# Optimization experiments

Measured on AMD Instinct MI355X. Metric: run time of the kernel, lower is better.

## Reference

```python
import jax, jax.numpy as jnp
import numpy as np

B = 512      # batch
T = 32       # time steps -> T-1 = 31 recurrent steps
Tm1 = T - 1
D = 256      # input_size (exogenous features)
HE = 512     # encoder hidden
HD = 512     # decoder hidden


def setup_inputs() -> dict:
    key = jax.random.key(0)
    ks = jax.random.split(key, 24)
    n = lambda k, shape, s=0.05: jax.random.normal(k, shape, dtype=jnp.float32) * s
    return dict(
        inputs=jax.random.normal(ks[0], (B, Tm1, D + 1), dtype=jnp.float32),
        enc_Wih=n(ks[1], (4 * HE, D)), enc_Whh=n(ks[2], (4 * HE, HE)),
        enc_bih=n(ks[3], (4 * HE,)), enc_bhh=n(ks[4], (4 * HE,)),
        enc_Wc=n(ks[5], (Tm1, 2 * HE)), enc_bc=n(ks[6], (Tm1,)),
        enc_Wd=n(ks[7], (Tm1, Tm1)), enc_bd=n(ks[8], (Tm1,)),
        enc_Wa=n(ks[9], (1, Tm1)), enc_ba=n(ks[10], (1,)),
        dec_W1=n(ks[11], (HE, 2 * HD + HE)), dec_b1=n(ks[12], (HE,)),
        dec_W2=n(ks[13], (1, HE)), dec_b2=n(ks[14], (1,)),
        dec_Wih=n(ks[15], (4 * HD, 1)), dec_Whh=n(ks[16], (4 * HD, HD)),
        dec_bih=n(ks[17], (4 * HD,)), dec_bhh=n(ks[18], (4 * HD,)),
        fc_W=n(ks[19], (1, HE + 1), 1.0),  # torch code does fc.weight.data.normal_() (std=1)
        fc_b=n(ks[20], (1,)),
        fcf_W=n(ks[21], (1, HD + HE)), fcf_b=n(ks[22], (1,)),
    )


def _lstm_step(x, h, c, Wih, Whh, bih, bhh):
    # single-step PyTorch LSTM; gate order i, f, g, o
    g = x @ Wih.T + bih + h @ Whh.T + bhh
    i, f, gg, o = jnp.split(g, 4, axis=-1)
    c2 = jax.nn.sigmoid(f) * c + jax.nn.sigmoid(i) * jnp.tanh(gg)
    return jax.nn.sigmoid(o) * jnp.tanh(c2), c2


def reference(inputs, enc_Wih, enc_Whh, enc_bih, enc_bhh, enc_Wc, enc_bc,
              enc_Wd, enc_bd, enc_Wa, enc_ba, dec_W1, dec_b1, dec_W2, dec_b2,
              dec_Wih, dec_Whh, dec_bih, dec_bhh, fc_W, fc_b, fcf_W, fcf_b):
    Bn = inputs.shape[0]
    y_hist = inputs[:, :, :1]   # idx_target = 0 -> [B, Tm1, 1]
    X = inputs[:, :, 1:]        # [B, Tm1, D]

    # linear_data(input_data.permute(0,2,1)) is time-invariant: [B, D, Tm1]
    t2 = jnp.einsum('btd,st->bds', X, enc_Wd) + enc_bd

    # ---- Encoder: input attention + LSTM over Tm1 steps ----
    def enc_step(carry, x_t):
        h, c = carry  # [B, HE] each
        # hidden/state are identical per input feature -> compute linear_concat once
        t1 = jnp.concatenate([h, c], axis=-1) @ enc_Wc.T + enc_bc        # [B, Tm1]
        score = jnp.tanh(t1[:, None, :] + t2) @ enc_Wa[0] + enc_ba[0]     # [B, D]
        attn = jax.nn.softmax(score, axis=1)
        w = attn * x_t                                                    # [B, D]
        h2, c2 = _lstm_step(w, h, c, enc_Wih, enc_Whh, enc_bih, enc_bhh)
        return (h2, c2), h2

    h0 = jnp.zeros((Bn, HE), dtype=inputs.dtype)
    (_, _), enc_h = jax.lax.scan(enc_step, (h0, h0), jnp.swapaxes(X, 0, 1))
    enc_out = jnp.swapaxes(enc_h, 0, 1)  # [B, Tm1, HE]

    # ---- Decoder: temporal attention + LSTM over Tm1 steps ----
    def dec_step(carry, y_t):
        h, c, _ = carry
        hs = jnp.concatenate([h, c], axis=-1)  # [B, 2*HD]
        x = jnp.concatenate(
            [jnp.broadcast_to(hs[:, None, :], (Bn, Tm1, 2 * HD)), enc_out], axis=-1)
        score = jnp.tanh(x @ dec_W1.T + dec_b1) @ dec_W2[0] + dec_b2[0]   # [B, Tm1]
        a = jax.nn.softmax(score, axis=1)
        ctx = jnp.einsum('bt,bte->be', a, enc_out)                        # [B, HE]
        y_tilde = jnp.concatenate([ctx, y_t], axis=-1) @ fc_W.T + fc_b    # [B, 1]
        h2, c2 = _lstm_step(y_tilde, h, c, dec_Wih, dec_Whh, dec_bih, dec_bhh)
        return (h2, c2, ctx), None

    hd0 = jnp.zeros((Bn, HD), dtype=inputs.dtype)
    ctx0 = jnp.zeros((Bn, HE), dtype=inputs.dtype)
    (hT, _, ctxT), _ = jax.lax.scan(dec_step, (hd0, hd0, ctx0),
                                    jnp.swapaxes(y_hist, 0, 1))
    return jnp.concatenate([hT, ctxT], axis=-1) @ fcf_W.T + fcf_b  # [B, 1]
```

## Files before the change

### kernel.cpp

```cpp
#include <hip/hip_runtime.h>
#include <math.h>

#define BATCH 512
#define TM1   31
#define DIMD  256

typedef _Float16 f16;
typedef _Float16 half2v __attribute__((ext_vector_type(2)));
typedef _Float16 half8 __attribute__((ext_vector_type(8)));
typedef float floatx16 __attribute__((ext_vector_type(16)));

__device__ __forceinline__ float sigmf(float x) { return 1.f / (1.f + __expf(-x)); }

__device__ __forceinline__ float tanh_fast(float x) {
    float ax = fabsf(x);
    float t  = __expf(-2.f * ax);
    float r  = (1.f - t) / (1.f + t);
    return copysignf(r, x);
}

__device__ __forceinline__ float blockReduceSum256(float v, float* sred) {
#pragma unroll
    for (int m = 32; m > 0; m >>= 1) v += __shfl_xor(v, m);
    __syncthreads();
    if ((threadIdx.x & 63) == 0) sred[threadIdx.x >> 6] = v;
    __syncthreads();
    return sred[0] + sred[1] + sred[2] + sred[3];
}

__device__ __forceinline__ float blockReduceMax256(float v, float* sred) {
#pragma unroll
    for (int m = 32; m > 0; m >>= 1) v = fmaxf(v, __shfl_xor(v, m));
    __syncthreads();
    if ((threadIdx.x & 63) == 0) sred[threadIdx.x >> 6] = v;
    __syncthreads();
    return fmaxf(fmaxf(sred[0], sred[1]), fmaxf(sred[2], sred[3]));
}

__global__ __launch_bounds__(256) void prep_t2s_kernel(
    const float* __restrict__ inputs,
    const float* __restrict__ eWih, const float* __restrict__ eWhh,
    const float* __restrict__ ebih, const float* __restrict__ ebhh,
    const float* __restrict__ dW1,  const float* __restrict__ dWhh,
    const float* __restrict__ dbih, const float* __restrict__ dbhh,
    const float* __restrict__ Wd,   const float* __restrict__ bd,
    const float* __restrict__ Wc,
    f16* __restrict__ eWf, f16* __restrict__ dWcf, f16* __restrict__ Vwf,
    float* __restrict__ ebcomb, float* __restrict__ dbias,
    f16* __restrict__ t2s, f16* __restrict__ Wcf)
{
    __shared__ float sX[TM1 * DIMD];
    __shared__ float sWd[TM1 * TM1];
    int b = blockIdx.x, tid = threadIdx.x;
    int idx = b * 256 + tid;
    const int stride = 512 * 256;

    for (int i = tid; i < TM1 * DIMD; i += 256) {
        int tt = i >> 8, d = i & 255;
        sX[i] = inputs[((size_t)b * TM1 + tt) * 257 + 1 + d];
    }
    for (int i = tid; i < TM1 * TM1; i += 256) sWd[i] = Wd[i];
    __syncthreads();
    int d = tid;
    for (int s = 0; s < TM1; s++) {
        float acc = bd[s];
        for (int tt = 0; tt < TM1; tt++) acc += sX[tt * DIMD + d] * sWd[s * TM1 + tt];
        t2s[((size_t)b * TM1 + s) * DIMD + d] = (f16)acc;
    }

    for (int g = idx; g < 2048 * 96; g += stride) {
        int n = g / 96, k0 = (g % 96) * 8;
        const float* src = (k0 < 256) ? (eWih + n * 256 + k0)
                                      : (eWhh + n * 512 + (k0 - 256));
        float4 v0 = *(const float4*)src;
        float4 v1 = *(const float4*)(src + 4);
        f16 h[8] = {(f16)v0.x, (f16)v0.y, (f16)v0.z, (f16)v0.w,
                    (f16)v1.x, (f16)v1.y, (f16)v1.z, (f16)v1.w};
        *(half8*)(eWf + n * 768 + k0) = *(half8*)h;
    }
    for (int g = idx; g < 2560 * 128; g += stride) {
        int n = g >> 7, k0 = (g & 127) * 8;
        float vv[8] = {};
        if (n < 512) {
            const float* src = dW1 + n * 1536 + k0;
            float4 v0 = *(const float4*)src, v1 = *(const float4*)(src + 4);
            vv[0]=v0.x; vv[1]=v0.y; vv[2]=v0.z; vv[3]=v0.w;
            vv[4]=v1.x; vv[5]=v1.y; vv[6]=v1.z; vv[7]=v1.w;
        } else if (k0 < 512) {
            const float* src = dWhh + (n - 512) * 512 + k0;
            float4 v0 = *(const float4*)src, v1 = *(const float4*)(src + 4);
            vv[0]=v0.x; vv[1]=v0.y; vv[2]=v0.z; vv[3]=v0.w;
            vv[4]=v1.x; vv[5]=v1.y; vv[6]=v1.z; vv[7]=v1.w;
        }
        f16 h[8];
#pragma unroll
        for (int e = 0; e < 8; e++) h[e] = (f16)vv[e];
        *(half8*)(dWcf + n * 1024 + k0) = *(half8*)h;
    }
    for (int g = idx; g < 512 * 64; g += stride) {
        int n = g >> 6, k0 = (g & 63) * 8;
        const float* src = dW1 + n * 1536 + 1024 + k0;
        float4 v0 = *(const float4*)src, v1 = *(const float4*)(src + 4);
        f16 h[8] = {(f16)v0.x, (f16)v0.y, (f16)v0.z, (f16)v0.w,
                    (f16)v1.x, (f16)v1.y, (f16)v1.z, (f16)v1.w};
        *(half8*)(Vwf + n * 512 + k0) = *(half8*)h;
    }
    for (int g = idx; g < 3968; g += stride) {
        int k0 = g * 8;
        float4 v0 = *(const float4*)(Wc + k0);
        float4 v1 = *(const float4*)(Wc + k0 + 4);
        f16 h[8] = {(f16)v0.x, (f16)v0.y, (f16)v0.z, (f16)v0.w,
                    (f16)v1.x, (f16)v1.y, (f16)v1.z, (f16)v1.w};
        *(half8*)(Wcf + k0) = *(half8*)h;
    }
    for (int i = idx; i < 2048; i += stride) ebcomb[i] = ebih[i] + ebhh[i];
    for (int i = idx; i < 2560; i += stride)
        dbias[i] = (i < 512) ? 0.f : (dbih[i - 512] + dbhh[i - 512]);
}

__global__ __launch_bounds__(256) void gemm1f(
    const f16* __restrict__ A, int lda,
    const f16* __restrict__ W, int ldw,
    const float* __restrict__ bias, f16* __restrict__ C, int ldc,
    long long Cstride, int K, int nsplit, int NT, int MT, int KS)
{
    __shared__ f16 sAh[64 * 128];
    __shared__ f16 sWh[64 * 128];
    int tid = threadIdx.x, bid = blockIdx.x;
    int nbase = bid % NT;
    int m0 = ((bid / NT) % MT) * 64;
    int ks = bid / (NT * MT);
    int lane = tid & 63, wid = tid >> 6;
    int wm = wid >> 1, wn = wid & 1;
    int rl = lane & 31, kq = lane >> 5;

    int sr = tid >> 2;
    int gb = (tid & 3) * 4;
    int st0 = sr * 128 + (((gb + 0) ^ (sr & 15)) * 8);
    int st1 = sr * 128 + (((gb + 1) ^ (sr & 15)) * 8);
    int st2 = sr * 128 + (((gb + 2) ^ (sr & 15)) * 8);
    int st3 = sr * 128 + (((gb + 3) ^ (sr & 15)) * 8);
    int arow = (wm * 32 + rl) * 128;
    int wrow = (wn * 32 + rl) * 128;
    int swk = rl & 15;

    int n0 = nbase * 64;
    int Kfull = (n0 >= nsplit) ? 512 : K;
    int ksz = Kfull / KS;
    int kbeg = ks * ksz, kend = kbeg + ksz;

    const f16* pA = A + (size_t)(m0 + sr) * lda + gb * 8;
    const f16* pW = W + (size_t)(n0 + sr) * ldw + gb * 8;

    float4 rA0 = *(const float4*)(pA + kbeg);
    float4 rA1 = *(const float4*)(pA + kbeg + 8);
    float4 rA2 = *(const float4*)(pA + kbeg + 16);
    float4 rA3 = *(const float4*)(pA + kbeg + 24);
    float4 rW0 = *(const float4*)(pW + kbeg);
    float4 rW1 = *(const float4*)(pW + kbeg + 8);
    float4 rW2 = *(const float4*)(pW + kbeg + 16);
    float4 rW3 = *(const float4*)(pW + kbeg + 24);

    floatx16 acc = {};
    for (int k0 = kbeg; k0 < kend; k0 += 128) {
        __syncthreads();
        *(float4*)&sAh[st0] = rA0; *(float4*)&sAh[st1] = rA1;
        *(float4*)&sAh[st2] = rA2; *(float4*)&sAh[st3] = rA3;
        *(float4*)&sWh[st0] = rW0; *(float4*)&sWh[st1] = rW1;
        *(float4*)&sWh[st2] = rW2; *(float4*)&sWh[st3] = rW3;
        __syncthreads();
        int kn = k0 + 128;
        if (kn < kend) {
            rA0 = *(const float4*)(pA + kn);      rA1 = *(const float4*)(pA + kn + 8);
            rA2 = *(const float4*)(pA + kn + 16); rA3 = *(const float4*)(pA + kn + 24);
            rW0 = *(const float4*)(pW + kn);      rW1 = *(const float4*)(pW + kn + 8);
            rW2 = *(const float4*)(pW + kn + 16); rW3 = *(const float4*)(pW + kn + 24);
        }
#pragma unroll
        for (int kk = 0; kk < 128; kk += 16) {
            int lg = (kk >> 3) + kq;
            half8 ah = *(const half8*)&sAh[arow + ((lg ^ swk) * 8)];
            half8 wh = *(const half8*)&sWh[wrow + ((lg ^ swk) * 8)];
            acc = __builtin_amdgcn_mfma_f32_32x32x16_f16(ah, wh, acc, 0, 0, 0);
        }
    }

    int col = n0 + wn * 32 + rl;
    float bv = (ks == 0) ? bias[col] : 0.f;
    f16* Cp = C + (size_t)ks * Cstride;
#pragma unroll
    for (int rr = 0; rr < 16; ++rr) {
        int row = m0 + wm * 32 + (rr & 3) + 8 * (rr >> 2) + 4 * kq;
        Cp[(size_t)row * ldc + col] = (f16)(acc[rr] + bv);
    }
}

__global__ __launch_bounds__(256) void gemm_v(
    const f16* __restrict__ A, int lda,
    const f16* __restrict__ W, int ldw,
    const float* __restrict__ bias, f16* __restrict__ C, int ldc,
    int K, int NT, int MT, int NREP)
{
    __shared__ f16 sAh[64 * 64];
    __shared__ f16 sWh[64 * 64];
    int tid = threadIdx.x, bid = blockIdx.x;
    int nbase = bid % NT;
    int m0 = ((bid / NT) % MT) * 64;
    int lane = tid & 63, wid = tid >> 6;
    int wm = wid >> 1, wn = wid & 1;
    int rl = lane & 31, kq = lane >> 5;
    int sr = tid >> 2;
    int g0 = (tid & 3) * 2;
    int s0 = sr * 64 + ((g0 ^ (sr & 7)) * 8);
    int s1 = sr * 64 + (((g0 + 1) ^ (sr & 7)) * 8);
    int arow = (wm * 32 + rl) * 64;
    int wrow = (wn * 32 + rl) * 64;
    int sw = (rl & 7);

    const f16* pA = A + (size_t)(m0 + sr) * lda + g0 * 8;

    for (int r = 0; r < NREP; ++r) {
        int n0 = (nbase + r * NT) * 64;
        const f16* pW = W + (size_t)(n0 + sr) * ldw + g0 * 8;
        float4 rA0 = *(const float4*)(pA);
        float4 rA1 = *(const float4*)(pA + 8);
        float4 rW0 = *(const float4*)(pW);
        float4 rW1 = *(const float4*)(pW + 8);
        floatx16 acc = {};
        for (int k0 = 0; k0 < K; k0 += 64) {
            __syncthreads();
            *(float4*)&sAh[s0] = rA0; *(float4*)&sAh[s1] = rA1;
            *(float4*)&sWh[s0] = rW0; *(float4*)&sWh[s1] = rW1;
            __syncthreads();
            int kn = k0 + 64;
            if (kn < K) {
                rA0 = *(const float4*)(pA + kn); rA1 = *(const float4*)(pA + kn + 8);
                rW0 = *(const float4*)(pW + kn); rW1 = *(const float4*)(pW + kn + 8);
            }
#pragma unroll
            for (int kk = 0; kk < 64; kk += 16) {
                int lg = (kk >> 3) + kq;
                int off = ((lg ^ sw) * 8);
                half8 ah = *(const half8*)&sAh[arow + off];
                half8 wh = *(const half8*)&sWh[wrow + off];
                acc = __builtin_amdgcn_mfma_f32_32x32x16_f16(ah, wh, acc, 0, 0, 0);
            }
        }
        int col = n0 + wn * 32 + rl;
        float bv = bias[col];
#pragma unroll
        for (int rr = 0; rr < 16; ++rr) {
            int row = m0 + wm * 32 + (rr & 3) + 8 * (rr >> 2) + 4 * kq;
            C[(size_t)row * ldc + col] = (f16)(acc[rr] + bv);
        }
    }
}

__global__ __launch_bounds__(256) void enc_step_kernel(
    const float* __restrict__ inputs, const f16* __restrict__ t2s,
    const f16* __restrict__ Wcf, const float* __restrict__ bc,
    const float* __restrict__ Wa, const float* __restrict__ ba,
    const f16* __restrict__ g, long long gstride,
    float* __restrict__ hc,
    f16* __restrict__ Ahi, f16* __restrict__ enchi,
    float* __restrict__ hc_dec, f16* __restrict__ hdhi,
    int t) {
    __shared__ float sh_hc[1024];
    __shared__ float t1s[32];
    __shared__ float sred[4];
    int b = blockIdx.x, tid = threadIdx.x;

    if (t > 0) {
        int e = tid * 2;
        const f16* gp = g + (size_t)b * 2048 + e;
        float gi0 = 0.f, gi1 = 0.f, gf0 = 0.f, gf1 = 0.f;
        float gg0 = 0.f, gg1 = 0.f, go0 = 0.f, go1 = 0.f;
#pragma unroll
        for (int s = 0; s < 2; s++) {
            const f16* q = gp + s * gstride;
            half2v a = *(const half2v*)(q);
            half2v f = *(const half2v*)(q + 512);
            half2v gv = *(const half2v*)(q + 1024);
            half2v o = *(const half2v*)(q + 1536);
            gi0 += (float)a[0]; gi1 += (float)a[1];
            gf0 += (float)f[0]; gf1 += (float)f[1];
            gg0 += (float)gv[0]; gg1 += (float)gv[1];
            go0 += (float)o[0]; go1 += (float)o[1];
        }
        float2 cpv = *(const float2*)(hc + b * 1024 + 512 + e);
        float c20 = sigmf(gf0) * cpv.x + sigmf(gi0) * tanh_fast(gg0);
        float c21 = sigmf(gf1) * cpv.y + sigmf(gi1) * tanh_fast(gg1);
        float h20 = sigmf(go0) * tanh_fast(c20);
        float h21 = sigmf(go1) * tanh_fast(c21);
        *(float2*)(hc + b * 1024 + e) = make_float2(h20, h21);
        *(float2*)(hc + b * 1024 + 512 + e) = make_float2(c20, c21);
        sh_hc[e] = h20; sh_hc[e + 1] = h21;
        sh_hc[512 + e] = c20; sh_hc[512 + e + 1] = c21;
        half2v hv; hv[0] = (f16)h20; hv[1] = (f16)h21;
        *(half2v*)(enchi + ((size_t)b * TM1 + (t - 1)) * 512 + e) = hv;
    } else {
        for (int j = tid; j < 1024; j += 256) { sh_hc[j] = 0.f; hc[b * 1024 + j] = 0.f; }
    }
    if (t == TM1) {
        for (int j = tid; j < 1024; j += 256) {
            hc_dec[b * 1024 + j] = 0.f;
            hdhi[b * 1024 + j] = (f16)0.f;
        }
        return;
    }
    __syncthreads();

    if (tid < 248) {
        int s = tid >> 3, l8 = tid & 7;
        const f16* wrow = Wcf + s * 1024;
        float p = 0.f;
        for (int j = l8 * 8; j < 1024; j += 64) {
            half8 w8 = *(const half8*)(wrow + j);
#pragma unroll
            for (int e = 0; e < 8; e++) p += (float)w8[e] * sh_hc[j + e];
        }
        p += __shfl_xor(p, 1); p += __shfl_xor(p, 2); p += __shfl_xor(p, 4);
        if (l8 == 0) t1s[s] = p + bc[s];
    }
    __syncthreads();

    int d = tid;
    float sc = ba[0];
    const f16* t2p = t2s + ((size_t)b * TM1) * DIMD + d;
    for (int s = 0; s < TM1; s++) sc += tanh_fast(t1s[s] + (float)t2p[s * DIMD]) * Wa[s];
    float mx = blockReduceMax256(sc, sred);
    float ex = __expf(sc - mx);
    float sm = blockReduceSum256(ex, sred);
    float w = (ex / sm) * inputs[((size_t)b * TM1 + t) * 257 + 1 + d];
    Ahi[b * 768 + d] = (f16)w;
    for (int j = tid; j < 512; j += 256)
        Ahi[b * 768 + 256 + j] = (f16)sh_hc[j];
}

__global__ __launch_bounds__(256) void dec_step_kernel(
    const float* __restrict__ inputs, const f16* __restrict__ V,
    const float* __restrict__ W2, const float* __restrict__ b2,
    const f16* __restrict__ enchi,
    const float* __restrict__ fcW, const float* __restrict__ fcb,
    const float* __restrict__ Wih,
    const f16* __restrict__ gu, long long ustride,
    float* __restrict__ hc, f16* __restrict__ hdhi,
    const float* __restrict__ fcfW, const float* __restrict__ fcfb,
    float* __restrict__ out, int t) {
    __shared__ float su[512];
    __shared__ float sw2[512];
    __shared__ float s_att[TM1];
    __shared__ float sred[4];
    int b = blockIdx.x, tid = threadIdx.x;
    const bool last = (t == TM1 - 1);
    {
        int e = tid * 2;
        const f16* q = gu + (size_t)b * 2560 + e;
        half2v a0 = *(const half2v*)(q);
        half2v a1 = *(const half2v*)(q + ustride);
        su[e]     = (float)a0[0] + (float)a1[0];
        su[e + 1] = (float)a0[1] + (float)a1[1];
        sw2[e] = W2[e]; sw2[e + 1] = W2[e + 1];
    }
    __syncthreads();
    if (tid < 248) {
        int tp = tid >> 3, l8 = tid & 7;
        const f16* vrow = V + ((size_t)b * TM1 + tp) * 512;
        float p = 0.f;
        for (int j = l8 * 8; j < 512; j += 64) {
            half8 v8 = *(const half8*)(vrow + j);
#pragma unroll
            for (int e = 0; e < 8; e++)
                p += tanh_fast(su[j + e] + (float)v8[e]) * sw2[j + e];
        }
        p += __shfl_xor(p, 1); p += __shfl_xor(p, 2); p += __shfl_xor(p, 4);
        if (l8 == 0) s_att[tp] = p + b2[0];
    }
    __syncthreads();
    if (tid < 64) {
        float v = (tid < TM1) ? s_att[tid] : -3.4e38f;
        float m = v;
#pragma unroll
        for (int k = 32; k > 0; k >>= 1) m = fmaxf(m, __shfl_xor(m, k));
        float e = (tid < TM1) ? __expf(v - m) : 0.f;
        float s = e;
#pragma unroll
        for (int k = 32; k > 0; k >>= 1) s += __shfl_xor(s, k);
        if (tid < TM1) s_att[tid] = e / s;
    }
    __syncthreads();

    float part = 0.f;
    float pctx = 0.f;
#pragma unroll
    for (int r = 0; r < 2; r++) {
        int e = tid + r * 256;
        float cx = 0.f;
        const f16* eh = enchi + (size_t)b * TM1 * 512 + e;
        for (int tp = 0; tp < TM1; tp++)
            cx += s_att[tp] * (float)eh[tp * 512];
        part += cx * fcW[e];
        if (last) pctx += cx * fcfW[512 + e];
    }
    float y = inputs[((size_t)b * TM1 + t) * 257];
    float ysum = blockReduceSum256(part, sred);
    float y_til = ysum + y * fcW[512] + fcb[0];

    float ph = 0.f;
    {
        int e = tid * 2;
        const f16* q = gu + (size_t)b * 2560 + e;
        float gi0 = 0.f, gi1 = 0.f, gf0 = 0.f, gf1 = 0.f;
        float gg0 = 0.f, gg1 = 0.f, go0 = 0.f, go1 = 0.f;
#pragma unroll
        for (int s = 0; s < 2; s++) {
            const f16* qq = q + s * ustride;
            half2v a = *(const half2v*)(qq + 512);
            half2v f = *(const half2v*)(qq + 1024);
            half2v gv = *(const half2v*)(qq + 1536);
            half2v o = *(const half2v*)(qq + 2048);
            gi0 += (float)a[0]; gi1 += (float)a[1];
            gf0 += (float)f[0]; gf1 += (float)f[1];
            gg0 += (float)gv[0]; gg1 += (float)gv[1];
            go0 += (float)o[0]; go1 += (float)o[1];
        }
        gi0 += y_til * Wih[e];        gi1 += y_til * Wih[e + 1];
        gf0 += y_til * Wih[512 + e];  gf1 += y_til * Wih[512 + e + 1];
        gg0 += y_til * Wih[1024 + e]; gg1 += y_til * Wih[1024 + e + 1];
        go0 += y_til * Wih[1536 + e]; go1 += y_til * Wih[1536 + e + 1];
        float2 cpv = *(const float2*)(hc + b * 1024 + 512 + e);
        float c20 = sigmf(gf0) * cpv.x + sigmf(gi0) * tanh_fast(gg0);
        float c21 = sigmf(gf1) * cpv.y + sigmf(gi1) * tanh_fast(gg1);
        float h20 = sigmf(go0) * tanh_fast(c20);
        float h21 = sigmf(go1) * tanh_fast(c21);
        if (!last) {
            *(float2*)(hc + b * 1024 + e) = make_float2(h20, h21);
            *(float2*)(hc + b * 1024 + 512 + e) = make_float2(c20, c21);
            half2v hv; hv[0] = (f16)h20; hv[1] = (f16)h21;
            half2v cv; cv[0] = (f16)c20; cv[1] = (f16)c21;
            *(half2v*)(hdhi + (size_t)b * 1024 + e) = hv;
            *(half2v*)(hdhi + (size_t)b * 1024 + 512 + e) = cv;
        } else {
            ph += h20 * fcfW[e] + h21 * fcfW[e + 1];
        }
    }
    if (last) {
        float s = blockReduceSum256(ph + pctx, sred);
        if (tid == 0) out[b] = s + fcfb[0];
    }
}

extern "C" void kernel_launch(void* const* d_in, const int* in_sizes, int n_in,
                              void* d_out, int out_size, void* d_ws, size_t ws_size,
                              hipStream_t stream) {
    const float* inputs  = (const float*)d_in[0];
    const float* eWih    = (const float*)d_in[1];
    const float* eWhh    = (const float*)d_in[2];
    const float* ebih    = (const float*)d_in[3];
    const float* ebhh    = (const float*)d_in[4];
    const float* eWc     = (const float*)d_in[5];
    const float* ebc     = (const float*)d_in[6];
    const float* eWd     = (const float*)d_in[7];
    const float* ebd     = (const float*)d_in[8];
    const float* eWa     = (const float*)d_in[9];
    const float* eba     = (const float*)d_in[10];
    const float* dW1     = (const float*)d_in[11];
    const float* db1     = (const float*)d_in[12];
    const float* dW2     = (const float*)d_in[13];
    const float* db2     = (const float*)d_in[14];
    const float* dWih    = (const float*)d_in[15];
    const float* dWhh    = (const float*)d_in[16];
    const float* dbih    = (const float*)d_in[17];
    const float* dbhh    = (const float*)d_in[18];
    const float* fcW     = (const float*)d_in[19];
    const float* fcb     = (const float*)d_in[20];
    const float* fcfW    = (const float*)d_in[21];
    const float* fcfb    = (const float*)d_in[22];
    float* out = (float*)d_out;

    float* scr = (float*)d_ws;
    f16* t2s = (f16*)scr;
    f16* Vf  = (f16*)scr;
    f16* g0e = (f16*)(scr + 4063232);
    f16* gu0 = (f16*)(scr + 4063232);
    float* hc_enc = scr + 6684672;
    f16*   Ahi    = (f16*)(scr + 7208960);
    float* hc_dec = scr + 7405568;
    f16*   hdhi   = (f16*)(scr + 7929856);
    f16* fp = (f16*)(scr + 8192000);
    f16* eWf   = fp;             fp += 1572864;
    f16* dWcf  = fp;             fp += 2621440;
    f16* Vwf   = fp;             fp += 262144;
    f16* enchi = fp;             fp += 8126464;
    float* ebcomb = (float*)(((uintptr_t)fp + 15) & ~(uintptr_t)15);
    float* dbias  = ebcomb + 2048;
    f16* Wcf = (f16*)(dbias + 2560);

    hipLaunchKernelGGL(prep_t2s_kernel, dim3(512), dim3(256), 0, stream,
                       inputs, eWih, eWhh, ebih, ebhh, dW1, dWhh, dbih, dbhh,
                       eWd, ebd, eWc, eWf, dWcf, Vwf,
                       ebcomb, dbias, t2s, Wcf);

    const long long gstride = 1048576;
    const long long ustride = 1310720;

    for (int t = 0; t < TM1; t++) {
        hipLaunchKernelGGL(enc_step_kernel, dim3(BATCH), dim3(256), 0, stream,
                           inputs, t2s, Wcf, ebc, eWa, eba, g0e, gstride, hc_enc,
                           Ahi, enchi, hc_dec, hdhi, t);
        hipLaunchKernelGGL(gemm1f, dim3(512), dim3(256), 0, stream,
                           Ahi, 768, eWf, 768, ebcomb,
                           g0e, 2048, gstride, 768, 1 << 30, 32, 8, 2);
    }
    hipLaunchKernelGGL(enc_step_kernel, dim3(BATCH), dim3(256), 0, stream,
                       inputs, t2s, Wcf, ebc, eWa, eba, g0e, gstride, hc_enc,
                       Ahi, enchi, hc_dec, hdhi, TM1);

    hipLaunchKernelGGL(gemm_v, dim3(992), dim3(256), 0, stream,
                       enchi, 512, Vwf, 512, db1,
                       Vf, 512, 512, 4, 248, 2);

    for (int t = 0; t < TM1; t++) {
        hipLaunchKernelGGL(gemm1f, dim3(640), dim3(256), 0, stream,
                           hdhi, 1024, dWcf, 1024, dbias,
                           gu0, 2560, ustride, 1024, 512, 40, 8, 2);
        hipLaunchKernelGGL(dec_step_kernel, dim3(BATCH), dim3(256), 0, stream,
                           inputs, Vf, dW2, db2, enchi, fcW, fcb, dWih,
                           gu0, ustride, hc_dec, hdhi, fcfW, fcfb, out, t);
    }
}
```

Baseline: 1.445 ms.

## Widen prep grid, drop unused h stores, vectorize f16 loads and stores

The prep kernel now launches 2048 blocks, with only the first 512 computing t2s and all blocks sharing the weight-conversion loops, so conversion gets more parallelism. The encoder and decoder step kernels stop writing the fp32 h half of their hc state, which appears unused, and only zero the c half. The Ahi hidden copy and the decoder context loop now use half2 vector loads and stores with float2 weight loads. Correctness relies on nothing else reading the fp32 h values.

```diff
diff --git a/kernel.cpp b/kernel.cpp
--- a/kernel.cpp
+++ b/kernel.cpp
@@ -53,19 +53,21 @@
     __shared__ float sWd[TM1 * TM1];
     int b = blockIdx.x, tid = threadIdx.x;
     int idx = b * 256 + tid;
-    const int stride = 512 * 256;
-
-    for (int i = tid; i < TM1 * DIMD; i += 256) {
-        int tt = i >> 8, d = i & 255;
-        sX[i] = inputs[((size_t)b * TM1 + tt) * 257 + 1 + d];
-    }
-    for (int i = tid; i < TM1 * TM1; i += 256) sWd[i] = Wd[i];
-    __syncthreads();
-    int d = tid;
-    for (int s = 0; s < TM1; s++) {
-        float acc = bd[s];
-        for (int tt = 0; tt < TM1; tt++) acc += sX[tt * DIMD + d] * sWd[s * TM1 + tt];
-        t2s[((size_t)b * TM1 + s) * DIMD + d] = (f16)acc;
+    const int stride = gridDim.x * 256;
+
+    if (b < 512) {
+        for (int i = tid; i < TM1 * DIMD; i += 256) {
+            int tt = i >> 8, d = i & 255;
+            sX[i] = inputs[((size_t)b * TM1 + tt) * 257 + 1 + d];
+        }
+        for (int i = tid; i < TM1 * TM1; i += 256) sWd[i] = Wd[i];
+        __syncthreads();
+        int d = tid;
+        for (int s = 0; s < TM1; s++) {
+            float acc = bd[s];
+            for (int tt = 0; tt < TM1; tt++) acc += sX[tt * DIMD + d] * sWd[s * TM1 + tt];
+            t2s[((size_t)b * TM1 + s) * DIMD + d] = (f16)acc;
+        }
     }
 
     for (int g = idx; g < 2048 * 96; g += stride) {
@@ -292,20 +294,18 @@
         float c21 = sigmf(gf1) * cpv.y + sigmf(gi1) * tanh_fast(gg1);
         float h20 = sigmf(go0) * tanh_fast(c20);
         float h21 = sigmf(go1) * tanh_fast(c21);
-        *(float2*)(hc + b * 1024 + e) = make_float2(h20, h21);
         *(float2*)(hc + b * 1024 + 512 + e) = make_float2(c20, c21);
         sh_hc[e] = h20; sh_hc[e + 1] = h21;
         sh_hc[512 + e] = c20; sh_hc[512 + e + 1] = c21;
         half2v hv; hv[0] = (f16)h20; hv[1] = (f16)h21;
         *(half2v*)(enchi + ((size_t)b * TM1 + (t - 1)) * 512 + e) = hv;
     } else {
-        for (int j = tid; j < 1024; j += 256) { sh_hc[j] = 0.f; hc[b * 1024 + j] = 0.f; }
+        for (int j = tid; j < 1024; j += 256) { sh_hc[j] = 0.f; }
+        for (int j = tid; j < 512; j += 256) hc[b * 1024 + 512 + j] = 0.f;
     }
     if (t == TM1) {
-        for (int j = tid; j < 1024; j += 256) {
-            hc_dec[b * 1024 + j] = 0.f;
-            hdhi[b * 1024 + j] = (f16)0.f;
-        }
+        for (int j = tid; j < 512; j += 256) hc_dec[b * 1024 + 512 + j] = 0.f;
+        for (int j = tid; j < 1024; j += 256) hdhi[b * 1024 + j] = (f16)0.f;
         return;
     }
     __syncthreads();
@@ -333,8 +333,11 @@
     float sm = blockReduceSum256(ex, sred);
     float w = (ex / sm) * inputs[((size_t)b * TM1 + t) * 257 + 1 + d];
     Ahi[b * 768 + d] = (f16)w;
-    for (int j = tid; j < 512; j += 256)
-        Ahi[b * 768 + 256 + j] = (f16)sh_hc[j];
+    {
+        int j = tid * 2;
+        half2v hv; hv[0] = (f16)sh_hc[j]; hv[1] = (f16)sh_hc[j + 1];
+        *(half2v*)(Ahi + b * 768 + 256 + j) = hv;
+    }
 }
 
 __global__ __launch_bounds__(256) void dec_step_kernel(
@@ -390,17 +393,22 @@
     }
     __syncthreads();
 
-    float part = 0.f;
-    float pctx = 0.f;
-#pragma unroll
-    for (int r = 0; r < 2; r++) {
-        int e = tid + r * 256;
-        float cx = 0.f;
+    float part, pctx = 0.f;
+    {
+        int e = tid * 2;
+        float cx0 = 0.f, cx1 = 0.f;
         const f16* eh = enchi + (size_t)b * TM1 * 512 + e;
-        for (int tp = 0; tp < TM1; tp++)
-            cx += s_att[tp] * (float)eh[tp * 512];
-        part += cx * fcW[e];
-        if (last) pctx += cx * fcfW[512 + e];
+        for (int tp = 0; tp < TM1; tp++) {
+            half2v v2 = *(const half2v*)(eh + tp * 512);
+            cx0 += s_att[tp] * (float)v2[0];
+            cx1 += s_att[tp] * (float)v2[1];
+        }
+        float2 fw = *(const float2*)(fcW + e);
+        part = cx0 * fw.x + cx1 * fw.y;
+        if (last) {
+            float2 fw2 = *(const float2*)(fcfW + 512 + e);
+            pctx = cx0 * fw2.x + cx1 * fw2.y;
+        }
     }
     float y = inputs[((size_t)b * TM1 + t) * 257];
     float ysum = blockReduceSum256(part, sred);
@@ -434,7 +442,6 @@
         float h20 = sigmf(go0) * tanh_fast(c20);
         float h21 = sigmf(go1) * tanh_fast(c21);
         if (!last) {
-            *(float2*)(hc + b * 1024 + e) = make_float2(h20, h21);
             *(float2*)(hc + b * 1024 + 512 + e) = make_float2(c20, c21);
             half2v hv; hv[0] = (f16)h20; hv[1] = (f16)h21;
             half2v cv; cv[0] = (f16)c20; cv[1] = (f16)c21;
@@ -496,7 +503,7 @@
     float* dbias  = ebcomb + 2048;
     f16* Wcf = (f16*)(dbias + 2560);
 
-    hipLaunchKernelGGL(prep_t2s_kernel, dim3(512), dim3(256), 0, stream,
+    hipLaunchKernelGGL(prep_t2s_kernel, dim3(2048), dim3(256), 0, stream,
                        inputs, eWih, eWhh, ebih, ebhh, dW1, dWhh, dbih, dbhh,
                        eWd, ebd, eWc, eWf, dWcf, Vwf,
                        ebcomb, dbias, t2s, Wcf);
```

Result: no change. 1.441 ms (-0.3%).
